# Performance work log

Hardware: AMD Instinct MI355X
Metric: run time of the kernel (lower is better)

Reference implementation:

```python
import jax, jax.numpy as jnp
import numpy as np

NUM_HEADS = 8
CHUNK = 64
DIM = 1024


def setup_inputs() -> dict:
    key = jax.random.key(0)
    ks = jax.random.split(key, 5)
    B, C, L = 8, DIM, 4096
    scale = 1.0 / np.sqrt(C)
    x = jax.random.normal(ks[0], (B, C, L), dtype=jnp.float32)
    # Weights stored as [in, out] so y = x @ W + b (equiv. to torch Linear with W_t = W.T)
    Wq = jax.random.normal(ks[1], (C, C), dtype=jnp.float32) * scale
    Wk = jax.random.normal(ks[2], (C, C), dtype=jnp.float32) * scale
    Wv = jax.random.normal(ks[3], (C, C), dtype=jnp.float32) * scale
    Wo = jax.random.normal(ks[4], (C, C), dtype=jnp.float32) * scale
    z = jnp.zeros((C,), dtype=jnp.float32)
    return {"x": x, "Wq": Wq, "bq": z, "Wk": Wk, "bk": z, "Wv": Wv, "bv": z, "Wo": Wo, "bo": z}


def reference(x, Wq, bq, Wk, bk, Wv, bv, Wo, bo):
    B, C, L = x.shape
    H = NUM_HEADS
    hd = C // H
    nc = L // CHUNK  # number of chunks (L divisible by CHUNK)
    sqrt_d = jnp.asarray(np.sqrt(hd), dtype=x.dtype)

    xt = jnp.transpose(x, (0, 2, 1))  # [B, L, C]
    # Projections -> [B, nc, chunk, H, hd]
    Q = (xt @ Wq + bq).reshape(B, nc, CHUNK, H, hd)
    K = (xt @ Wk + bk).reshape(B, nc, CHUNK, H, hd)
    V = (xt @ Wv + bv).reshape(B, nc, CHUNK, H, hd)

    # Block-diagonal attention: each chunk attends only within itself
    scores = jnp.einsum('bnqhd,bnkhd->bnhqk', Q, K) / sqrt_d  # [B, nc, H, ck, ck]
    attn = jax.nn.softmax(scores, axis=-1)
    out = jnp.einsum('bnhqk,bnkhd->bnqhd', attn, V)  # [B, nc, ck, H, hd]

    out = out.reshape(B, L, C)
    out = out @ Wo + bo  # output projection
    return jnp.transpose(out, (0, 2, 1))  # [B, C, L]
```

## Files before the change

kernel.cpp:

```cpp
#include <hip/hip_runtime.h>

typedef __attribute__((ext_vector_type(8))) short short8;
typedef __attribute__((ext_vector_type(8))) unsigned short us8;
typedef __attribute__((ext_vector_type(4))) float f32x4;

#define C_DIM 1024
#define L_DIM 4096
#define B_DIM 8
#define H_DIM 8
#define HD 128
#define CHUNK 64

__device__ inline unsigned short bf16_hi(float f) {
    unsigned u = __float_as_uint(f);
    unsigned r = (u + 0x7FFFu + ((u >> 16) & 1u)) >> 16;
    return (unsigned short)r;
}
__device__ inline us8 pack8(float4 a, float4 b) {
    us8 v;
    v[0] = bf16_hi(a.x); v[1] = bf16_hi(a.y); v[2] = bf16_hi(a.z); v[3] = bf16_hi(a.w);
    v[4] = bf16_hi(b.x); v[5] = bf16_hi(b.y); v[6] = bf16_hi(b.z); v[7] = bf16_hi(b.w);
    return v;
}

__global__ void split_w(const float* __restrict__ W, unsigned short* __restrict__ Wt) {
    __shared__ float tile[32][33];
    int nb = blockIdx.x * 32;
    int kb = blockIdx.y * 32;
    for (int i = 0; i < 4; ++i)
        tile[threadIdx.y + i * 8][threadIdx.x] =
            W[(size_t)(kb + threadIdx.y + i * 8) * C_DIM + nb + threadIdx.x];
    __syncthreads();
    for (int i = 0; i < 4; ++i) {
        int n = nb + threadIdx.y + i * 8;
        int k = kb + threadIdx.x;
        float v = tile[threadIdx.x][threadIdx.y + i * 8];
        Wt[(size_t)n * C_DIM + k] = bf16_hi(v);
    }
}

__global__ __launch_bounds__(256) void split_x(const float* __restrict__ x,
                                               unsigned short* __restrict__ xsp, int b0) {
    __shared__ float tile[64][65];
    int t = threadIdx.x;
    int lb = blockIdx.x * 64, cb = blockIdx.y * 64, bp = blockIdx.z;
    const float* xp = x + ((size_t)(b0 + bp) * C_DIM + cb) * L_DIM + lb;
#pragma unroll
    for (int p = 0; p < 4; ++p) {
        int cr = p * 16 + (t >> 4);
        int lo4 = (t & 15) * 4;
        float4 v = *(const float4*)&xp[(size_t)cr * L_DIM + lo4];
        tile[lo4 + 0][cr] = v.x;
        tile[lo4 + 1][cr] = v.y;
        tile[lo4 + 2][cr] = v.z;
        tile[lo4 + 3][cr] = v.w;
    }
    __syncthreads();
#pragma unroll
    for (int p = 0; p < 2; ++p) {
        int l = p * 32 + (t >> 3);
        int c8 = (t & 7) * 8;
        us8 hv;
#pragma unroll
        for (int i = 0; i < 8; ++i)
            hv[i] = bf16_hi(tile[l][c8 + i]);
        size_t row = (size_t)bp * L_DIM + lb + l;
        *(us8*)&xsp[row * C_DIM + cb + c8] = hv;
    }
}

#define TM 128
#define TN 128
#define BK 64
#define LDSS 72

__global__ __launch_bounds__(256) void gemm_bf16(
    const unsigned short* __restrict__ A,
    const unsigned short* __restrict__ Bt,
    const float* __restrict__ bias,
    float* __restrict__ Y,
    int M, int N, int K, int tmode, int b0)
{
    __shared__ unsigned short As[TM * LDSS];
    __shared__ unsigned short Bs[TN * LDSS];
    int t = threadIdx.x;
    int m0 = blockIdx.y * TM, n0 = blockIdx.x * TN;
    int wave = t >> 6, lane = t & 63;
    int wr = wave >> 1, wc = wave & 1;
    int lm = lane & 15, quad = lane >> 4;

    f32x4 acc[4][4];
    for (int i = 0; i < 4; ++i)
        for (int j = 0; j < 4; ++j) { f32x4 z = {0.f, 0.f, 0.f, 0.f}; acc[i][j] = z; }

    const int lrow = t >> 3;
    const int lk = (t & 7) * 8;

    for (int kt = 0; kt < K; kt += BK) {
#pragma unroll
        for (int p = 0; p < 4; ++p) {
            int r = p * 32 + lrow;
            *(us8*)&As[r * LDSS + lk] = *(const us8*)&A[(size_t)(m0 + r) * K + kt + lk];
            *(us8*)&Bs[r * LDSS + lk] = *(const us8*)&Bt[(size_t)(n0 + r) * K + kt + lk];
        }
        __syncthreads();
#pragma unroll
        for (int s = 0; s < 2; ++s) {
            short8 af[4], bfr[4];
#pragma unroll
            for (int i = 0; i < 4; ++i)
                af[i] = *(const short8*)&As[(wr * 64 + i * 16 + lm) * LDSS + s * 32 + quad * 8];
#pragma unroll
            for (int j = 0; j < 4; ++j)
                bfr[j] = *(const short8*)&Bs[(wc * 64 + j * 16 + lm) * LDSS + s * 32 + quad * 8];
#pragma unroll
            for (int i = 0; i < 4; ++i)
#pragma unroll
                for (int j = 0; j < 4; ++j)
                    acc[i][j] = __builtin_amdgcn_mfma_f32_16x16x32_bf16(af[i], bfr[j], acc[i][j], 0, 0, 0);
        }
        __syncthreads();
    }

    if (tmode == 0) {
#pragma unroll
        for (int i = 0; i < 4; ++i) {
            int row = m0 + wr * 64 + i * 16 + quad * 4;
#pragma unroll
            for (int j = 0; j < 4; ++j) {
                int col = n0 + wc * 64 + j * 16 + lm;
                float b = bias[col];
#pragma unroll
                for (int r = 0; r < 4; ++r)
                    Y[(size_t)(row + r) * N + col] = acc[i][j][r] + b;
            }
        }
    } else {
#pragma unroll
        for (int i = 0; i < 4; ++i) {
            int row = m0 + wr * 64 + i * 16 + quad * 4;
            int bp = row >> 12;
            int l = row & (L_DIM - 1);
#pragma unroll
            for (int j = 0; j < 4; ++j) {
                int col = n0 + wc * 64 + j * 16 + lm;
                float b = bias[col];
                float4 v;
                v.x = acc[i][j][0] + b; v.y = acc[i][j][1] + b;
                v.z = acc[i][j][2] + b; v.w = acc[i][j][3] + b;
                *(float4*)&Y[((size_t)(b0 + bp) * N + col) * L_DIM + l] = v;
            }
        }
    }
}

__global__ __launch_bounds__(256) void attn(
    const float* __restrict__ Qt, const float* __restrict__ Kt, const float* __restrict__ Vt,
    unsigned short* __restrict__ Osp)
{
    __shared__ __align__(16) char smem[53248];
    unsigned short* Qs = (unsigned short*)smem;
    unsigned short* Ks = (unsigned short*)(smem + 17408);
    unsigned short* Vs = (unsigned short*)(smem + 34816);
    float* Ss = (float*)smem;
    unsigned short* Ps = (unsigned short*)(smem + 17408);
    float* Os = (float*)smem;

    int t = threadIdx.x;
    int idx = blockIdx.x;
    int h = idx & 7;
    int chunk = (idx >> 3) & 63;
    int bp = idx >> 9;
    size_t rowbase = (size_t)bp * L_DIM + (size_t)chunk * CHUNK;
    const float* Qp = Qt + rowbase * C_DIM + h * HD;
    const float* Kp = Kt + rowbase * C_DIM + h * HD;
    const float* Vp = Vt + ((size_t)bp * C_DIM + h * HD) * L_DIM + (size_t)chunk * CHUNK;
    int wave = t >> 6, lane = t & 63;
    int lm = lane & 15, quad = lane >> 4;

#pragma unroll
    for (int p = 0; p < 4; ++p) {
        int row = p * 16 + (t >> 4);
        int c8 = (t & 15) * 8;
        float4 a = *(const float4*)&Qp[(size_t)row * C_DIM + c8];
        float4 b = *(const float4*)&Qp[(size_t)row * C_DIM + c8 + 4];
        *(us8*)&Qs[row * 136 + c8] = pack8(a, b);
        a = *(const float4*)&Kp[(size_t)row * C_DIM + c8];
        b = *(const float4*)&Kp[(size_t)row * C_DIM + c8 + 4];
        *(us8*)&Ks[row * 136 + c8] = pack8(a, b);
    }
#pragma unroll
    for (int p = 0; p < 4; ++p) {
        int row = p * 32 + (t >> 3);
        int c8 = (t & 7) * 8;
        float4 a = *(const float4*)&Vp[(size_t)row * L_DIM + c8];
        float4 b = *(const float4*)&Vp[(size_t)row * L_DIM + c8 + 4];
        *(us8*)&Vs[row * 72 + c8] = pack8(a, b);
    }
    __syncthreads();

    f32x4 sa[4];
#pragma unroll
    for (int i = 0; i < 4; ++i) { f32x4 z = {0.f, 0.f, 0.f, 0.f}; sa[i] = z; }
#pragma unroll
    for (int ks = 0; ks < 4; ++ks) {
        short8 bfr = *(const short8*)&Ks[(wave * 16 + lm) * 136 + ks * 32 + quad * 8];
#pragma unroll
        for (int i = 0; i < 4; ++i) {
            short8 af = *(const short8*)&Qs[(i * 16 + lm) * 136 + ks * 32 + quad * 8];
            sa[i] = __builtin_amdgcn_mfma_f32_16x16x32_bf16(af, bfr, sa[i], 0, 0, 0);
        }
    }
    __syncthreads();

    const float scale = 0.08838834764831845f;
#pragma unroll
    for (int i = 0; i < 4; ++i)
#pragma unroll
        for (int r = 0; r < 4; ++r)
            Ss[(i * 16 + quad * 4 + r) * 68 + wave * 16 + lm] = sa[i][r] * scale;
    __syncthreads();

    {
        int srow = t >> 2, scb = (t & 3) * 16;
        float v[16];
        float mx = -1e30f;
#pragma unroll
        for (int q = 0; q < 4; ++q) {
            float4 f = *(const float4*)&Ss[srow * 68 + scb + q * 4];
            v[q * 4 + 0] = f.x; v[q * 4 + 1] = f.y; v[q * 4 + 2] = f.z; v[q * 4 + 3] = f.w;
            mx = fmaxf(fmaxf(fmaxf(mx, f.x), fmaxf(f.y, f.z)), f.w);
        }
        mx = fmaxf(mx, __shfl_xor(mx, 1));
        mx = fmaxf(mx, __shfl_xor(mx, 2));
        float sum = 0.f;
#pragma unroll
        for (int i = 0; i < 16; ++i) { v[i] = __expf(v[i] - mx); sum += v[i]; }
        sum += __shfl_xor(sum, 1);
        sum += __shfl_xor(sum, 2);
        float inv = 1.0f / sum;
        us8 p0, p1;
#pragma unroll
        for (int i = 0; i < 8; ++i) {
            p0[i] = bf16_hi(v[i] * inv);
            p1[i] = bf16_hi(v[8 + i] * inv);
        }
        *(us8*)&Ps[srow * 72 + scb] = p0;
        *(us8*)&Ps[srow * 72 + scb + 8] = p1;
    }
    __syncthreads();

    f32x4 oa[4][2];
#pragma unroll
    for (int i = 0; i < 4; ++i)
#pragma unroll
        for (int j = 0; j < 2; ++j) { f32x4 z = {0.f, 0.f, 0.f, 0.f}; oa[i][j] = z; }
#pragma unroll
    for (int ks = 0; ks < 2; ++ks) {
        short8 bv0 = *(const short8*)&Vs[(wave * 32 + lm) * 72 + ks * 32 + quad * 8];
        short8 bv1 = *(const short8*)&Vs[(wave * 32 + 16 + lm) * 72 + ks * 32 + quad * 8];
#pragma unroll
        for (int i = 0; i < 4; ++i) {
            short8 af = *(const short8*)&Ps[(i * 16 + lm) * 72 + ks * 32 + quad * 8];
            oa[i][0] = __builtin_amdgcn_mfma_f32_16x16x32_bf16(af, bv0, oa[i][0], 0, 0, 0);
            oa[i][1] = __builtin_amdgcn_mfma_f32_16x16x32_bf16(af, bv1, oa[i][1], 0, 0, 0);
        }
    }
    __syncthreads();

#pragma unroll
    for (int i = 0; i < 4; ++i)
#pragma unroll
        for (int j = 0; j < 2; ++j)
#pragma unroll
            for (int r = 0; r < 4; ++r)
                Os[(i * 16 + quad * 4 + r) * 132 + wave * 32 + j * 16 + lm] = oa[i][j][r];
    __syncthreads();

    {
        int row = t >> 2, dstart = (t & 3) * 32;
        size_t obase = (rowbase + row) * C_DIM + h * HD + dstart;
#pragma unroll
        for (int c = 0; c < 4; ++c) {
            us8 hv;
#pragma unroll
            for (int i = 0; i < 8; ++i)
                hv[i] = bf16_hi(Os[row * 132 + dstart + c * 8 + i]);
            *(us8*)&Osp[obase + c * 8] = hv;
        }
    }
}

extern "C" void kernel_launch(void* const* d_in, const int* in_sizes, int n_in,
                              void* d_out, int out_size, void* d_ws, size_t ws_size,
                              hipStream_t stream) {
    const float* x  = (const float*)d_in[0];
    const float* Wq = (const float*)d_in[1];
    const float* bq = (const float*)d_in[2];
    const float* Wk = (const float*)d_in[3];
    const float* bk = (const float*)d_in[4];
    const float* Wv = (const float*)d_in[5];
    const float* bv = (const float*)d_in[6];
    const float* Wo = (const float*)d_in[7];
    const float* bo = (const float*)d_in[8];
    float* out = (float*)d_out;

    const size_t MB = 1024ull * 1024ull;
    char* base = (char*)d_ws;
    unsigned short* WspQ = (unsigned short*)(base + 0 * 2 * MB);
    unsigned short* WspK = (unsigned short*)(base + 1 * 2 * MB);
    unsigned short* WspV = (unsigned short*)(base + 2 * 2 * MB);
    unsigned short* WspO = (unsigned short*)(base + 3 * 2 * MB);

    int BG = 8;
    while (BG > 1 && 16 * MB + (size_t)BG * 56 * MB > ws_size) BG >>= 1;

    char* p = base + 16 * MB;
    unsigned short* xsp = (unsigned short*)p;
    float* Qt = (float*)(p + (size_t)BG * 8 * MB);
    float* Kt = (float*)(p + (size_t)BG * 24 * MB);
    float* Vt = (float*)(p + (size_t)BG * 40 * MB);

    dim3 tb(32, 8);
    split_w<<<dim3(32, 32), tb, 0, stream>>>(Wq, WspQ);
    split_w<<<dim3(32, 32), tb, 0, stream>>>(Wk, WspK);
    split_w<<<dim3(32, 32), tb, 0, stream>>>(Wv, WspV);
    split_w<<<dim3(32, 32), tb, 0, stream>>>(Wo, WspO);

    for (int b0 = 0; b0 < B_DIM; b0 += BG) {
        int M = BG * L_DIM;
        split_x<<<dim3(L_DIM / 64, C_DIM / 64, BG), 256, 0, stream>>>(x, xsp, b0);
        dim3 gg(C_DIM / TN, M / TM);
        gemm_bf16<<<gg, 256, 0, stream>>>(xsp, WspQ, bq, Qt, M, C_DIM, C_DIM, 0, 0);
        gemm_bf16<<<gg, 256, 0, stream>>>(xsp, WspK, bk, Kt, M, C_DIM, C_DIM, 0, 0);
        gemm_bf16<<<gg, 256, 0, stream>>>(xsp, WspV, bv, Vt, M, C_DIM, C_DIM, 1, 0);
        attn<<<BG * (L_DIM / CHUNK) * H_DIM, 256, 0, stream>>>(Qt, Kt, Vt, xsp);
        gemm_bf16<<<gg, 256, 0, stream>>>(xsp, WspO, bo, out, M, C_DIM, C_DIM, 1, b0);
    }
}
```

Baseline: 801.3 us.

## Store Q/K/V projections as bf16 and swizzle GEMM workgroup order

The Q/K/V projection GEMMs now round their outputs to bf16 in the epilogue and write 16-bit values, and the attention kernel loads them directly without converting. This halves the intermediate write and read traffic and shrinks the workspace, so a larger batch group fits. Separately, the GEMM remaps block IDs in groups of eight, which changes which tiles run together and may improve cache locality. The bf16 epilogue writes are scalar 2-byte stores, which could be less efficient than the previous float stores.

```diff
diff --git a/kernel.cpp b/kernel.cpp
--- a/kernel.cpp
+++ b/kernel.cpp
@@ -15,12 +15,6 @@
     unsigned u = __float_as_uint(f);
     unsigned r = (u + 0x7FFFu + ((u >> 16) & 1u)) >> 16;
     return (unsigned short)r;
-}
-__device__ inline us8 pack8(float4 a, float4 b) {
-    us8 v;
-    v[0] = bf16_hi(a.x); v[1] = bf16_hi(a.y); v[2] = bf16_hi(a.z); v[3] = bf16_hi(a.w);
-    v[4] = bf16_hi(b.x); v[5] = bf16_hi(b.y); v[6] = bf16_hi(b.z); v[7] = bf16_hi(b.w);
-    return v;
 }
 
 __global__ void split_w(const float* __restrict__ W, unsigned short* __restrict__ Wt) {
@@ -78,13 +72,22 @@
     const unsigned short* __restrict__ A,
     const unsigned short* __restrict__ Bt,
     const float* __restrict__ bias,
-    float* __restrict__ Y,
-    int M, int N, int K, int tmode, int b0)
+    void* __restrict__ Yv,
+    int M, int N, int K, int omode, int b0)
 {
     __shared__ unsigned short As[TM * LDSS];
     __shared__ unsigned short Bs[TN * LDSS];
     int t = threadIdx.x;
-    int m0 = blockIdx.y * TM, n0 = blockIdx.x * TN;
+
+    int nwg = gridDim.x * gridDim.y;
+    int bid = blockIdx.y * gridDim.x + blockIdx.x;
+    int bx, by;
+    if ((nwg & 7) == 0) {
+        int wg = (bid & 7) * (nwg >> 3) + (bid >> 3);
+        bx = wg % gridDim.x; by = wg / gridDim.x;
+    } else { bx = blockIdx.x; by = blockIdx.y; }
+
+    int m0 = by * TM, n0 = bx * TN;
     int wave = t >> 6, lane = t & 63;
     int wr = wave >> 1, wc = wave & 1;
     int lm = lane & 15, quad = lane >> 4;
@@ -122,7 +125,8 @@
         __syncthreads();
     }
 
-    if (tmode == 0) {
+    if (omode == 0) {
+        float* Y = (float*)Yv;
 #pragma unroll
         for (int i = 0; i < 4; ++i) {
             int row = m0 + wr * 64 + i * 16 + quad * 4;
@@ -135,7 +139,22 @@
                     Y[(size_t)(row + r) * N + col] = acc[i][j][r] + b;
             }
         }
-    } else {
+    } else if (omode == 2) {
+        unsigned short* Y = (unsigned short*)Yv;
+#pragma unroll
+        for (int i = 0; i < 4; ++i) {
+            int row = m0 + wr * 64 + i * 16 + quad * 4;
+#pragma unroll
+            for (int j = 0; j < 4; ++j) {
+                int col = n0 + wc * 64 + j * 16 + lm;
+                float b = bias[col];
+#pragma unroll
+                for (int r = 0; r < 4; ++r)
+                    Y[(size_t)(row + r) * N + col] = bf16_hi(acc[i][j][r] + b);
+            }
+        }
+    } else if (omode == 1) {
+        float* Y = (float*)Yv;
 #pragma unroll
         for (int i = 0; i < 4; ++i) {
             int row = m0 + wr * 64 + i * 16 + quad * 4;
@@ -151,11 +170,29 @@
                 *(float4*)&Y[((size_t)(b0 + bp) * N + col) * L_DIM + l] = v;
             }
         }
+    } else {
+        unsigned short* Y = (unsigned short*)Yv;
+#pragma unroll
+        for (int i = 0; i < 4; ++i) {
+            int row = m0 + wr * 64 + i * 16 + quad * 4;
+            int bp = row >> 12;
+            int l = row & (L_DIM - 1);
+#pragma unroll
+            for (int j = 0; j < 4; ++j) {
+                int col = n0 + wc * 64 + j * 16 + lm;
+                float b = bias[col];
+                ushort4 v;
+                v.x = bf16_hi(acc[i][j][0] + b); v.y = bf16_hi(acc[i][j][1] + b);
+                v.z = bf16_hi(acc[i][j][2] + b); v.w = bf16_hi(acc[i][j][3] + b);
+                *(ushort4*)&Y[((size_t)(b0 + bp) * N + col) * L_DIM + l] = v;
+            }
+        }
     }
 }
 
 __global__ __launch_bounds__(256) void attn(
-    const float* __restrict__ Qt, const float* __restrict__ Kt, const float* __restrict__ Vt,
+    const unsigned short* __restrict__ Qt, const unsigned short* __restrict__ Kt,
+    const unsigned short* __restrict__ Vt,
     unsigned short* __restrict__ Osp)
 {
     __shared__ __align__(16) char smem[53248];
@@ -172,30 +209,24 @@
     int chunk = (idx >> 3) & 63;
     int bp = idx >> 9;
     size_t rowbase = (size_t)bp * L_DIM + (size_t)chunk * CHUNK;
-    const float* Qp = Qt + rowbase * C_DIM + h * HD;
-    const float* Kp = Kt + rowbase * C_DIM + h * HD;
-    const float* Vp = Vt + ((size_t)bp * C_DIM + h * HD) * L_DIM + (size_t)chunk * CHUNK;
+    const unsigned short* Qp = Qt + rowbase * C_DIM + h * HD;
+    const unsigned short* Kp = Kt + rowbase * C_DIM + h * HD;
+    const unsigned short* Vp = Vt + ((size_t)bp * C_DIM + h * HD) * L_DIM + (size_t)chunk * CHUNK;
     int wave = t >> 6, lane = t & 63;
     int lm = lane & 15, quad = lane >> 4;
 
 #pragma unroll
     for (int p = 0; p < 4; ++p) {
-        int row = p * 16 + (t >> 4);
-        int c8 = (t & 15) * 8;
-        float4 a = *(const float4*)&Qp[(size_t)row * C_DIM + c8];
-        float4 b = *(const float4*)&Qp[(size_t)row * C_DIM + c8 + 4];
-        *(us8*)&Qs[row * 136 + c8] = pack8(a, b);
-        a = *(const float4*)&Kp[(size_t)row * C_DIM + c8];
-        b = *(const float4*)&Kp[(size_t)row * C_DIM + c8 + 4];
-        *(us8*)&Ks[row * 136 + c8] = pack8(a, b);
+        int f = p * 256 + t;
+        int row = f >> 4, c8 = (f & 15) * 8;
+        *(us8*)&Qs[row * 136 + c8] = *(const us8*)&Qp[(size_t)row * C_DIM + c8];
+        *(us8*)&Ks[row * 136 + c8] = *(const us8*)&Kp[(size_t)row * C_DIM + c8];
     }
 #pragma unroll
     for (int p = 0; p < 4; ++p) {
-        int row = p * 32 + (t >> 3);
-        int c8 = (t & 7) * 8;
-        float4 a = *(const float4*)&Vp[(size_t)row * L_DIM + c8];
-        float4 b = *(const float4*)&Vp[(size_t)row * L_DIM + c8 + 4];
-        *(us8*)&Vs[row * 72 + c8] = pack8(a, b);
+        int f = p * 256 + t;
+        int row = f >> 3, c8 = (f & 7) * 8;
+        *(us8*)&Vs[row * 72 + c8] = *(const us8*)&Vp[(size_t)row * L_DIM + c8];
     }
     __syncthreads();
 
@@ -313,13 +344,13 @@
     unsigned short* WspO = (unsigned short*)(base + 3 * 2 * MB);
 
     int BG = 8;
-    while (BG > 1 && 16 * MB + (size_t)BG * 56 * MB > ws_size) BG >>= 1;
+    while (BG > 1 && 16 * MB + (size_t)BG * 32 * MB > ws_size) BG >>= 1;
 
     char* p = base + 16 * MB;
     unsigned short* xsp = (unsigned short*)p;
-    float* Qt = (float*)(p + (size_t)BG * 8 * MB);
-    float* Kt = (float*)(p + (size_t)BG * 24 * MB);
-    float* Vt = (float*)(p + (size_t)BG * 40 * MB);
+    unsigned short* Qtb = (unsigned short*)(p + (size_t)BG * 8 * MB);
+    unsigned short* Ktb = (unsigned short*)(p + (size_t)BG * 16 * MB);
+    unsigned short* Vtb = (unsigned short*)(p + (size_t)BG * 24 * MB);
 
     dim3 tb(32, 8);
     split_w<<<dim3(32, 32), tb, 0, stream>>>(Wq, WspQ);
@@ -331,10 +362,10 @@
         int M = BG * L_DIM;
         split_x<<<dim3(L_DIM / 64, C_DIM / 64, BG), 256, 0, stream>>>(x, xsp, b0);
         dim3 gg(C_DIM / TN, M / TM);
-        gemm_bf16<<<gg, 256, 0, stream>>>(xsp, WspQ, bq, Qt, M, C_DIM, C_DIM, 0, 0);
-        gemm_bf16<<<gg, 256, 0, stream>>>(xsp, WspK, bk, Kt, M, C_DIM, C_DIM, 0, 0);
-        gemm_bf16<<<gg, 256, 0, stream>>>(xsp, WspV, bv, Vt, M, C_DIM, C_DIM, 1, 0);
-        attn<<<BG * (L_DIM / CHUNK) * H_DIM, 256, 0, stream>>>(Qt, Kt, Vt, xsp);
+        gemm_bf16<<<gg, 256, 0, stream>>>(xsp, WspQ, bq, Qtb, M, C_DIM, C_DIM, 2, 0);
+        gemm_bf16<<<gg, 256, 0, stream>>>(xsp, WspK, bk, Ktb, M, C_DIM, C_DIM, 2, 0);
+        gemm_bf16<<<gg, 256, 0, stream>>>(xsp, WspV, bv, Vtb, M, C_DIM, C_DIM, 3, 0);
+        attn<<<BG * (L_DIM / CHUNK) * H_DIM, 256, 0, stream>>>(Qtb, Ktb, Vtb, xsp);
         gemm_bf16<<<gg, 256, 0, stream>>>(xsp, WspO, bo, out, M, C_DIM, C_DIM, 1, b0);
     }
 }
```

Result: faster. 696.9 us (-13.0%).
